# Performance work log

Hardware: AMD Instinct MI355X
Metric: run time of the kernel (lower is better)

Reference implementation:

```python
import jax, jax.numpy as jnp
import numpy as np

# ---- O(2) irrep machinery -------------------------------------------------
# Irrep (m, p): dim = 1 if m == 0 else 2 (real basis (cos m*theta, sin m*theta)).
# Product rules from trig identities; 'component' normalization: cg *= sqrt(dim_out).
R2 = 1.0 / np.sqrt(2.0)

def _cg_paths(m1, p1, m2, p2):
    out = []
    if m1 == 0 and m2 == 0:
        out.append((0, p1 * p2, np.ones((1, 1, 1))))
    elif m1 == 0:
        c = np.zeros((1, 2, 2)); c[0, 0, 0] = 1.0; c[0, 1, 1] = 1.0
        out.append((m2, p1 * p2, c))
    elif m2 == 0:
        c = np.zeros((2, 1, 2)); c[0, 0, 0] = 1.0; c[1, 0, 1] = 1.0
        out.append((m1, p1 * p2, c))
    else:
        if m1 == m2:
            c = np.zeros((2, 2, 1)); c[0, 0, 0] = R2; c[1, 1, 0] = R2  # cos(a-b): scalar
            out.append((0, p1 * p2, c))
            c = np.zeros((2, 2, 1)); c[1, 0, 0] = R2; c[0, 1, 0] = -R2  # sin(a-b): pseudoscalar
            out.append((0, -p1 * p2, c))
        else:
            sgn = 1.0 if m1 > m2 else -1.0
            c = np.zeros((2, 2, 2))
            c[0, 0, 0] = R2; c[1, 1, 0] = R2          # cos(a-b) = cc + ss
            c[1, 0, 1] = sgn * R2; c[0, 1, 1] = -sgn * R2  # sin(a-b) = sc - cs
            out.append((abs(m1 - m2), p1 * p2, c))
        c = np.zeros((2, 2, 2))
        c[0, 0, 0] = R2; c[1, 1, 0] = -R2  # cos(a+b) = cc - ss
        c[1, 0, 1] = R2; c[0, 1, 1] = R2   # sin(a+b) = sc + cs
        out.append((m1 + m2, p1 * p2, c))
    # component normalization
    return [(m, p, (cg * np.sqrt(cg.shape[-1])).astype(np.float32)) for m, p, cg in out]

# (mul, m, parity) -- already regrouped (sorted, deduplicated)
IRREPS1 = [(64, 0, 1), (64, 1, 1), (64, 2, 1), (64, 3, 1)]  # dim 448
IRREPS2 = [(32, 0, 1), (32, 1, 1), (32, 2, 1)]              # dim 160

def _build():
    paths = []
    off1 = 0
    for mul1, m1, p1 in IRREPS1:
        d1 = 1 if m1 == 0 else 2
        off2 = 0
        for mul2, m2, p2 in IRREPS2:
            d2 = 1 if m2 == 0 else 2
            for mo, po, cg in _cg_paths(m1, p1, m2, p2):
                paths.append((off1, mul1, d1, off2, mul2, d2, cg, mo, po))
            off2 += mul2 * d2
        off1 += mul1 * d1
    # stable sort of output chunks by irrep (m, parity) -> irreps_out.sort().inv
    inv = sorted(range(len(paths)), key=lambda i: (paths[i][7], -paths[i][8]))
    return paths, inv

PATHS, INV = _build()
BATCH = 2048
DIM1 = 448
DIM2 = 160


def setup_inputs() -> dict:
    key = jax.random.key(0)
    k1, k2 = jax.random.split(key)
    return {
        "input1": jax.random.normal(k1, (BATCH, DIM1), dtype=jnp.float32),
        "input2": jax.random.normal(k2, (BATCH, DIM2), dtype=jnp.float32),
    }


def reference(input1, input2):
    # inputs already share leading shape and dtype (mirrors _prepare_inputs)
    lead = input1.shape[:-1]
    chunks = []
    for off1, mul1, d1, off2, mul2, d2, cg, _, _ in PATHS:
        x1 = input1[..., off1:off1 + mul1 * d1].reshape(lead + (mul1, d1))
        x2 = input2[..., off2:off2 + mul2 * d2].reshape(lead + (mul2, d2))
        cgj = jnp.asarray(cg, dtype=input1.dtype)  # (d1, d2, d_out), sparse CG
        chunk = jnp.einsum('...ui,...vj,ijk->...uvk', x1, x2, cgj)
        chunks.append(chunk.reshape(lead + (mul1 * mul2 * cg.shape[-1],)))
    return jnp.concatenate([chunks[i] for i in INV], axis=-1)
```

## Files before the change

### kernel.cpp

```cpp
#include <hip/hip_runtime.h>


#define R2F  0.70710678118654752440f
#define SQ2F 1.41421356237309504880f

constexpr int BATCH = 2048;
constexpr int DIM1  = 448;
constexpr int DIM2  = 160;
constexpr int ODIM  = 71680;

__global__ __launch_bounds__(256)
void tp_kernel(const float* __restrict__ g1, const float* __restrict__ g2,
               float* __restrict__ gout) {
    const int b  = blockIdx.x;
    const int t0 = threadIdx.x;

    __shared__ float s1[DIM1];
    __shared__ float s2[DIM2];
    {
        const float* x1 = g1 + (size_t)b * DIM1;
        const float* x2 = g2 + (size_t)b * DIM2;
        for (int i = t0; i < DIM1; i += 256) s1[i] = x1[i];
        for (int i = t0; i < DIM2; i += 256) s2[i] = x2[i];
    }
    __syncthreads();

    float4* out = (float4*)(gout + (size_t)b * ODIM);

    auto chunk_ss = [&](int dst4, const float* a, const float* b) {
#pragma unroll
        for (int r = 0; r < 2; ++r) {
            int t = t0 + r * 256;
            int u = t >> 3;
            int v = (4 * t) & 31;
            float au = a[u];
            out[dst4 + t] = make_float4(au * b[v], au * b[v + 1],
                                        au * b[v + 2], au * b[v + 3]);
        }
    };
    auto chunk_cos = [&](int dst4, const float* a, const float* b) {
#pragma unroll
        for (int r = 0; r < 2; ++r) {
            int t = t0 + r * 256;
            int u = t >> 3;
            int v = (4 * t) & 31;
            float ac = R2F * a[2 * u], as = R2F * a[2 * u + 1];
            float4 res;
            res.x = ac * b[2 * v + 0] + as * b[2 * v + 1];
            res.y = ac * b[2 * v + 2] + as * b[2 * v + 3];
            res.z = ac * b[2 * v + 4] + as * b[2 * v + 5];
            res.w = ac * b[2 * v + 6] + as * b[2 * v + 7];
            out[dst4 + t] = res;
        }
    };
    auto chunk_sin = [&](int dst4, const float* a, const float* b) {
#pragma unroll
        for (int r = 0; r < 2; ++r) {
            int t = t0 + r * 256;
            int u = t >> 3;
            int v = (4 * t) & 31;
            float ac = R2F * a[2 * u], as = R2F * a[2 * u + 1];
            float4 res;
            res.x = as * b[2 * v + 0] - ac * b[2 * v + 1];
            res.y = as * b[2 * v + 2] - ac * b[2 * v + 3];
            res.z = as * b[2 * v + 4] - ac * b[2 * v + 5];
            res.w = as * b[2 * v + 6] - ac * b[2 * v + 7];
            out[dst4 + t] = res;
        }
    };

    auto chunk_sv = [&](int dst4, const float* a, const float* b) {
#pragma unroll
        for (int r = 0; r < 4; ++r) {
            int t = t0 + r * 256;
            int u = t >> 4;
            int v = (2 * t) & 31;
            float au = SQ2F * a[u];
            out[dst4 + t] = make_float4(au * b[2 * v + 0], au * b[2 * v + 1],
                                        au * b[2 * v + 2], au * b[2 * v + 3]);
        }
    };
    auto chunk_vs = [&](int dst4, const float* a, const float* b) {
#pragma unroll
        for (int r = 0; r < 4; ++r) {
            int t = t0 + r * 256;
            int u = t >> 4;
            int v = (2 * t) & 31;
            float ac = SQ2F * a[2 * u], as = SQ2F * a[2 * u + 1];
            out[dst4 + t] = make_float4(ac * b[v], as * b[v],
                                        ac * b[v + 1], as * b[v + 1]);
        }
    };
    auto chunk_sum = [&](int dst4, const float* a, const float* b) {
#pragma unroll
        for (int r = 0; r < 4; ++r) {
            int t = t0 + r * 256;
            int u = t >> 4;
            int v = (2 * t) & 31;
            float ac = a[2 * u], as = a[2 * u + 1];
            float bc0 = b[2 * v + 0], bs0 = b[2 * v + 1];
            float bc1 = b[2 * v + 2], bs1 = b[2 * v + 3];
            out[dst4 + t] = make_float4(ac * bc0 - as * bs0, as * bc0 + ac * bs0,
                                        ac * bc1 - as * bs1, as * bc1 + ac * bs1);
        }
    };
    auto chunk_diff = [&](int dst4, const float* a, const float* b, float sgn) {
#pragma unroll
        for (int r = 0; r < 4; ++r) {
            int t = t0 + r * 256;
            int u = t >> 4;
            int v = (2 * t) & 31;
            float ac = a[2 * u], as = a[2 * u + 1];
            float bc0 = b[2 * v + 0], bs0 = b[2 * v + 1];
            float bc1 = b[2 * v + 2], bs1 = b[2 * v + 3];
            out[dst4 + t] = make_float4(ac * bc0 + as * bs0, sgn * (as * bc0 - ac * bs0),
                                        ac * bc1 + as * bs1, sgn * (as * bc1 - ac * bs1));
        }
    };

    chunk_ss  (    0, s1 +   0, s2 +  0);
    chunk_cos (  512, s1 +  64, s2 + 32);
    chunk_cos ( 1024, s1 + 192, s2 + 96);
    chunk_sin ( 1536, s1 +  64, s2 + 32);
    chunk_sin ( 2048, s1 + 192, s2 + 96);
    chunk_sv  ( 2560, s1 +   0, s2 + 32);
    chunk_vs  ( 3584, s1 +  64, s2 +  0);
    chunk_diff( 4608, s1 +  64, s2 + 96, -1.f);
    chunk_diff( 5632, s1 + 192, s2 + 32, +1.f);
    chunk_diff( 6656, s1 + 320, s2 + 96, +1.f);
    chunk_sv  ( 7680, s1 +   0, s2 + 96);
    chunk_sum ( 8704, s1 +  64, s2 + 32);
    chunk_vs  ( 9728, s1 + 192, s2 +  0);
    chunk_diff(10752, s1 + 320, s2 + 32, +1.f);
    chunk_sum (11776, s1 +  64, s2 + 96);
    chunk_sum (12800, s1 + 192, s2 + 32);
    chunk_vs  (13824, s1 + 320, s2 +  0);
    chunk_sum (14848, s1 + 192, s2 + 96);
    chunk_sum (15872, s1 + 320, s2 + 32);
    chunk_sum (16896, s1 + 320, s2 + 96);
}

extern "C" void kernel_launch(void* const* d_in, const int* in_sizes, int n_in,
                              void* d_out, int out_size, void* d_ws, size_t ws_size,
                              hipStream_t stream) {
    const float* x1 = (const float*)d_in[0];
    const float* x2 = (const float*)d_in[1];
    float* out = (float*)d_out;
    tp_kernel<<<BATCH, 256, 0, stream>>>(x1, x2, out);
}
```

Before: 576.3 us.

## Use nontemporal stores and regroup output chunks by shared input registers

```diff
diff --git a/kernel.cpp b/kernel.cpp
--- a/kernel.cpp
+++ b/kernel.cpp
@@ -8,6 +8,13 @@
 constexpr int DIM1  = 448;
 constexpr int DIM2  = 160;
 constexpr int ODIM  = 71680;
+
+typedef float v4f __attribute__((ext_vector_type(4)));
+
+__device__ __forceinline__ void ntst(v4f* p, float x, float y, float z, float w) {
+    v4f v = {x, y, z, w};
+    __builtin_nontemporal_store(v, p);
+}
 
 __global__ __launch_bounds__(256)
 void tp_kernel(const float* __restrict__ g1, const float* __restrict__ g2,
@@ -25,119 +32,148 @@
     }
     __syncthreads();
 
-    float4* out = (float4*)(gout + (size_t)b * ODIM);
+    v4f* out = (v4f*)(gout + (size_t)b * ODIM);
 
-    auto chunk_ss = [&](int dst4, const float* a, const float* b) {
+    const int us  = t0 >> 3;
+    const int vsc = (4 * t0) & 31;
+    const int vs2 = 2 * vsc;
+    const int uv  = t0 >> 4;
+    const int vv  = (2 * t0) & 31;
+    const int vv2 = 2 * vv;
+
+    {
+        float b0 = s2[vsc], b1 = s2[vsc + 1], b2 = s2[vsc + 2], b3 = s2[vsc + 3];
+        float a0 = s1[us], a1 = s1[us + 32];
+        ntst(out + t0,       a0*b0, a0*b1, a0*b2, a0*b3);
+        ntst(out + t0 + 256, a1*b0, a1*b1, a1*b2, a1*b3);
+    }
+
+    {
+        float av[4];
+#pragma unroll
+        for (int r = 0; r < 4; ++r) av[r] = s1[uv + 16 * r];
+        float p0 = SQ2F * s2[32 + vv2], p1 = SQ2F * s2[33 + vv2],
+              p2 = SQ2F * s2[34 + vv2], p3 = SQ2F * s2[35 + vv2];
+        float q0 = SQ2F * s2[96 + vv2], q1 = SQ2F * s2[97 + vv2],
+              q2 = SQ2F * s2[98 + vv2], q3 = SQ2F * s2[99 + vv2];
+#pragma unroll
+        for (int r = 0; r < 4; ++r) {
+            float a = av[r];
+            ntst(out + 2560 + t0 + 256 * r, a*p0, a*p1, a*p2, a*p3);
+            ntst(out + 7680 + t0 + 256 * r, a*q0, a*q1, a*q2, a*q3);
+        }
+    }
+
+    {
+        float ca[4], sa[4];
+#pragma unroll
+        for (int r = 0; r < 4; ++r) {
+            int j = 64 + 2 * (uv + 16 * r);
+            ca[r] = s1[j]; sa[r] = s1[j + 1];
+        }
+        float b00 = SQ2F * s2[vv], b01 = SQ2F * s2[vv + 1];
+        float b10 = s2[32 + vv2], b11 = s2[33 + vv2],
+              b12 = s2[34 + vv2], b13 = s2[35 + vv2];
+        float b20 = s2[96 + vv2], b21 = s2[97 + vv2],
+              b22 = s2[98 + vv2], b23 = s2[99 + vv2];
+#pragma unroll
+        for (int r = 0; r < 4; ++r) {
+            float c = ca[r], s = sa[r];
+            ntst(out + 3584 + t0 + 256 * r, c*b00, s*b00, c*b01, s*b01);
+            ntst(out + 4608 + t0 + 256 * r,
+                 c*b20 + s*b21, c*b21 - s*b20,
+                 c*b22 + s*b23, c*b23 - s*b22);
+            ntst(out + 8704 + t0 + 256 * r,
+                 c*b10 - s*b11, s*b10 + c*b11,
+                 c*b12 - s*b13, s*b12 + c*b13);
+            ntst(out + 11776 + t0 + 256 * r,
+                 c*b20 - s*b21, s*b20 + c*b21,
+                 c*b22 - s*b23, s*b22 + c*b23);
+        }
+        float e0 = s2[32 + vs2], e1 = s2[33 + vs2], e2 = s2[34 + vs2],
+              e3 = s2[35 + vs2], e4 = s2[36 + vs2], e5 = s2[37 + vs2],
+              e6 = s2[38 + vs2], e7 = s2[39 + vs2];
 #pragma unroll
         for (int r = 0; r < 2; ++r) {
-            int t = t0 + r * 256;
-            int u = t >> 3;
-            int v = (4 * t) & 31;
-            float au = a[u];
-            out[dst4 + t] = make_float4(au * b[v], au * b[v + 1],
-                                        au * b[v + 2], au * b[v + 3]);
+            int j = 64 + 2 * (us + 32 * r);
+            float c = R2F * s1[j], s = R2F * s1[j + 1];
+            ntst(out + 512 + t0 + 256 * r,
+                 c*e0 + s*e1, c*e2 + s*e3, c*e4 + s*e5, c*e6 + s*e7);
+            ntst(out + 1536 + t0 + 256 * r,
+                 s*e0 - c*e1, s*e2 - c*e3, s*e4 - c*e5, s*e6 - c*e7);
         }
-    };
-    auto chunk_cos = [&](int dst4, const float* a, const float* b) {
+    }
+
+    {
+        float ca[4], sa[4];
+#pragma unroll
+        for (int r = 0; r < 4; ++r) {
+            int j = 192 + 2 * (uv + 16 * r);
+            ca[r] = s1[j]; sa[r] = s1[j + 1];
+        }
+        float b00 = SQ2F * s2[vv], b01 = SQ2F * s2[vv + 1];
+        float b10 = s2[32 + vv2], b11 = s2[33 + vv2],
+              b12 = s2[34 + vv2], b13 = s2[35 + vv2];
+        float b20 = s2[96 + vv2], b21 = s2[97 + vv2],
+              b22 = s2[98 + vv2], b23 = s2[99 + vv2];
+#pragma unroll
+        for (int r = 0; r < 4; ++r) {
+            float c = ca[r], s = sa[r];
+            ntst(out + 5632 + t0 + 256 * r,
+                 c*b10 + s*b11, s*b10 - c*b11,
+                 c*b12 + s*b13, s*b12 - c*b13);
+            ntst(out + 9728 + t0 + 256 * r, c*b00, s*b00, c*b01, s*b01);
+            ntst(out + 12800 + t0 + 256 * r,
+                 c*b10 - s*b11, s*b10 + c*b11,
+                 c*b12 - s*b13, s*b12 + c*b13);
+            ntst(out + 14848 + t0 + 256 * r,
+                 c*b20 - s*b21, s*b20 + c*b21,
+                 c*b22 - s*b23, s*b22 + c*b23);
+        }
+        float e0 = s2[96 + vs2], e1 = s2[97 + vs2], e2 = s2[98 + vs2],
+              e3 = s2[99 + vs2], e4 = s2[100 + vs2], e5 = s2[101 + vs2],
+              e6 = s2[102 + vs2], e7 = s2[103 + vs2];
 #pragma unroll
         for (int r = 0; r < 2; ++r) {
-            int t = t0 + r * 256;
-            int u = t >> 3;
-            int v = (4 * t) & 31;
-            float ac = R2F * a[2 * u], as = R2F * a[2 * u + 1];
-            float4 res;
-            res.x = ac * b[2 * v + 0] + as * b[2 * v + 1];
-            res.y = ac * b[2 * v + 2] + as * b[2 * v + 3];
-            res.z = ac * b[2 * v + 4] + as * b[2 * v + 5];
-            res.w = ac * b[2 * v + 6] + as * b[2 * v + 7];
-            out[dst4 + t] = res;
+            int j = 192 + 2 * (us + 32 * r);
+            float c = R2F * s1[j], s = R2F * s1[j + 1];
+            ntst(out + 1024 + t0 + 256 * r,
+                 c*e0 + s*e1, c*e2 + s*e3, c*e4 + s*e5, c*e6 + s*e7);
+            ntst(out + 2048 + t0 + 256 * r,
+                 s*e0 - c*e1, s*e2 - c*e3, s*e4 - c*e5, s*e6 - c*e7);
         }
-    };
-    auto chunk_sin = [&](int dst4, const float* a, const float* b) {
-#pragma unroll
-        for (int r = 0; r < 2; ++r) {
-            int t = t0 + r * 256;
-            int u = t >> 3;
-            int v = (4 * t) & 31;
-            float ac = R2F * a[2 * u], as = R2F * a[2 * u + 1];
-            float4 res;
-            res.x = as * b[2 * v + 0] - ac * b[2 * v + 1];
-            res.y = as * b[2 * v + 2] - ac * b[2 * v + 3];
-            res.z = as * b[2 * v + 4] - ac * b[2 * v + 5];
-            res.w = as * b[2 * v + 6] - ac * b[2 * v + 7];
-            out[dst4 + t] = res;
-        }
-    };
+    }
 
-    auto chunk_sv = [&](int dst4, const float* a, const float* b) {
+    {
+        float ca[4], sa[4];
 #pragma unroll
         for (int r = 0; r < 4; ++r) {
-            int t = t0 + r * 256;
-            int u = t >> 4;
-            int v = (2 * t) & 31;
-            float au = SQ2F * a[u];
-            out[dst4 + t] = make_float4(au * b[2 * v + 0], au * b[2 * v + 1],
-                                        au * b[2 * v + 2], au * b[2 * v + 3]);
+            int j = 320 + 2 * (uv + 16 * r);
+            ca[r] = s1[j]; sa[r] = s1[j + 1];
         }
-    };
-    auto chunk_vs = [&](int dst4, const float* a, const float* b) {
+        float b00 = SQ2F * s2[vv], b01 = SQ2F * s2[vv + 1];
+        float b10 = s2[32 + vv2], b11 = s2[33 + vv2],
+              b12 = s2[34 + vv2], b13 = s2[35 + vv2];
+        float b20 = s2[96 + vv2], b21 = s2[97 + vv2],
+              b22 = s2[98 + vv2], b23 = s2[99 + vv2];
 #pragma unroll
         for (int r = 0; r < 4; ++r) {
-            int t = t0 + r * 256;
-            int u = t >> 4;
-            int v = (2 * t) & 31;
-            float ac = SQ2F * a[2 * u], as = SQ2F * a[2 * u + 1];
-            out[dst4 + t] = make_float4(ac * b[v], as * b[v],
-                                        ac * b[v + 1], as * b[v + 1]);
+            float c = ca[r], s = sa[r];
+            ntst(out + 6656 + t0 + 256 * r,
+                 c*b20 + s*b21, s*b20 - c*b21,
+                 c*b22 + s*b23, s*b22 - c*b23);
+            ntst(out + 10752 + t0 + 256 * r,
+                 c*b10 + s*b11, s*b10 - c*b11,
+                 c*b12 + s*b13, s*b12 - c*b13);
+            ntst(out + 13824 + t0 + 256 * r, c*b00, s*b00, c*b01, s*b01);
+            ntst(out + 15872 + t0 + 256 * r,
+                 c*b10 - s*b11, s*b10 + c*b11,
+                 c*b12 - s*b13, s*b12 + c*b13);
+            ntst(out + 16896 + t0 + 256 * r,
+                 c*b20 - s*b21, s*b20 + c*b21,
+                 c*b22 - s*b23, s*b22 + c*b23);
         }
-    };
-    auto chunk_sum = [&](int dst4, const float* a, const float* b) {
-#pragma unroll
-        for (int r = 0; r < 4; ++r) {
-            int t = t0 + r * 256;
-            int u = t >> 4;
-            int v = (2 * t) & 31;
-            float ac = a[2 * u], as = a[2 * u + 1];
-            float bc0 = b[2 * v + 0], bs0 = b[2 * v + 1];
-            float bc1 = b[2 * v + 2], bs1 = b[2 * v + 3];
-            out[dst4 + t] = make_float4(ac * bc0 - as * bs0, as * bc0 + ac * bs0,
-                                        ac * bc1 - as * bs1, as * bc1 + ac * bs1);
-        }
-    };
-    auto chunk_diff = [&](int dst4, const float* a, const float* b, float sgn) {
-#pragma unroll
-        for (int r = 0; r < 4; ++r) {
-            int t = t0 + r * 256;
-            int u = t >> 4;
-            int v = (2 * t) & 31;
-            float ac = a[2 * u], as = a[2 * u + 1];
-            float bc0 = b[2 * v + 0], bs0 = b[2 * v + 1];
-            float bc1 = b[2 * v + 2], bs1 = b[2 * v + 3];
-            out[dst4 + t] = make_float4(ac * bc0 + as * bs0, sgn * (as * bc0 - ac * bs0),
-                                        ac * bc1 + as * bs1, sgn * (as * bc1 - ac * bs1));
-        }
-    };
-
-    chunk_ss  (    0, s1 +   0, s2 +  0);
-    chunk_cos (  512, s1 +  64, s2 + 32);
-    chunk_cos ( 1024, s1 + 192, s2 + 96);
-    chunk_sin ( 1536, s1 +  64, s2 + 32);
-    chunk_sin ( 2048, s1 + 192, s2 + 96);
-    chunk_sv  ( 2560, s1 +   0, s2 + 32);
-    chunk_vs  ( 3584, s1 +  64, s2 +  0);
-    chunk_diff( 4608, s1 +  64, s2 + 96, -1.f);
-    chunk_diff( 5632, s1 + 192, s2 + 32, +1.f);
-    chunk_diff( 6656, s1 + 320, s2 + 96, +1.f);
-    chunk_sv  ( 7680, s1 +   0, s2 + 96);
-    chunk_sum ( 8704, s1 +  64, s2 + 32);
-    chunk_vs  ( 9728, s1 + 192, s2 +  0);
-    chunk_diff(10752, s1 + 320, s2 + 32, +1.f);
-    chunk_sum (11776, s1 +  64, s2 + 96);
-    chunk_sum (12800, s1 + 192, s2 + 32);
-    chunk_vs  (13824, s1 + 320, s2 +  0);
-    chunk_sum (14848, s1 + 192, s2 + 96);
-    chunk_sum (15872, s1 + 320, s2 + 32);
-    chunk_sum (16896, s1 + 320, s2 + 96);
+    }
 }
 
 extern "C" void kernel_launch(void* const* d_in, const int* in_sizes, int n_in,
```

After: 575.0 us. Within noise of the previous version (-0.2%).

## Split each row into per-piece blocks and use nontemporal stores

Applied to the files above, without the earlier changes.

```diff
diff --git a/kernel.cpp b/kernel.cpp
--- a/kernel.cpp
+++ b/kernel.cpp
@@ -4,140 +4,131 @@
 #define R2F  0.70710678118654752440f
 #define SQ2F 1.41421356237309504880f
 
-constexpr int BATCH = 2048;
-constexpr int DIM1  = 448;
-constexpr int DIM2  = 160;
-constexpr int ODIM  = 71680;
+constexpr int BATCH  = 2048;
+constexpr int DIM1   = 448;
+constexpr int DIM2   = 160;
+constexpr int ODIM   = 71680;
+constexpr int NPIECE = 35;
+
+typedef float v4f __attribute__((ext_vector_type(4)));
+
+__device__ __forceinline__ void ntst(v4f* p, float x, float y, float z, float w) {
+    v4f v = {x, y, z, w};
+    __builtin_nontemporal_store(v, p);
+}
+
+__constant__ const unsigned char PTYPE[NPIECE] = {
+    0, 1, 1, 2, 2,
+    3, 3, 4, 4, 6, 6, 7, 7, 7, 7,
+    3, 3, 5, 5, 4, 4, 7, 7,
+    5, 5, 5, 5, 4, 4,
+    5, 5, 5, 5,
+    5, 5
+};
+__constant__ const short AOFF[NPIECE] = {
+    0, 64, 192, 64, 192,
+    0, 0, 64, 64, 64, 64, 192, 192, 320, 320,
+    0, 0, 64, 64, 192, 192, 320, 320,
+    64, 64, 192, 192, 320, 320,
+    192, 192, 320, 320,
+    320, 320
+};
+__constant__ const short BOFF[NPIECE] = {
+    0, 32, 96, 32, 96,
+    32, 32, 0, 0, 96, 96, 32, 32, 96, 96,
+    96, 96, 32, 32, 0, 0, 32, 32,
+    96, 96, 32, 32, 0, 0,
+    96, 96, 32, 32,
+    96, 96
+};
+__constant__ const short UADD[NPIECE] = {
+    0, 0, 0, 0, 0,
+    0, 32, 0, 32, 0, 32, 0, 32, 0, 32,
+    0, 32, 0, 32, 0, 32, 0, 32,
+    0, 32, 0, 32, 0, 32,
+    0, 32, 0, 32,
+    0, 32
+};
 
 __global__ __launch_bounds__(256)
 void tp_kernel(const float* __restrict__ g1, const float* __restrict__ g2,
                float* __restrict__ gout) {
-    const int b  = blockIdx.x;
-    const int t0 = threadIdx.x;
+    const unsigned g   = blockIdx.x;
+    const unsigned row = g / NPIECE;
+    const int      p   = (int)(g - row * NPIECE);
+    const int      t0  = threadIdx.x;
 
-    __shared__ float s1[DIM1];
-    __shared__ float s2[DIM2];
-    {
-        const float* x1 = g1 + (size_t)b * DIM1;
-        const float* x2 = g2 + (size_t)b * DIM2;
-        for (int i = t0; i < DIM1; i += 256) s1[i] = x1[i];
-        for (int i = t0; i < DIM2; i += 256) s2[i] = x2[i];
+    const float* __restrict__ a  = g1 + (size_t)row * DIM1 + AOFF[p];
+    const float* __restrict__ bp = g2 + (size_t)row * DIM2 + BOFF[p];
+    v4f* out = (v4f*)(gout + (size_t)row * ODIM) + p * 512;
+
+    const int ty = PTYPE[p];
+
+    if (ty <= 2) {
+        const int v = (4 * t0) & 31;
+        const int u = t0 >> 3;
+        if (ty == 0) {
+            float b0 = bp[v], b1 = bp[v + 1], b2 = bp[v + 2], b3 = bp[v + 3];
+            float a0 = a[u], a1 = a[u + 32];
+            ntst(out + t0,       a0 * b0, a0 * b1, a0 * b2, a0 * b3);
+            ntst(out + t0 + 256, a1 * b0, a1 * b1, a1 * b2, a1 * b3);
+        } else {
+            const int v2 = 2 * v;
+            float e0 = bp[v2],     e1 = bp[v2 + 1], e2 = bp[v2 + 2], e3 = bp[v2 + 3],
+                  e4 = bp[v2 + 4], e5 = bp[v2 + 5], e6 = bp[v2 + 6], e7 = bp[v2 + 7];
+            float c0 = R2F * a[2 * u],        s0 = R2F * a[2 * u + 1];
+            float c1 = R2F * a[2 * u + 64],   s1 = R2F * a[2 * u + 65];
+            if (ty == 1) {
+                ntst(out + t0,       c0*e0 + s0*e1, c0*e2 + s0*e3,
+                                     c0*e4 + s0*e5, c0*e6 + s0*e7);
+                ntst(out + t0 + 256, c1*e0 + s1*e1, c1*e2 + s1*e3,
+                                     c1*e4 + s1*e5, c1*e6 + s1*e7);
+            } else {
+                ntst(out + t0,       s0*e0 - c0*e1, s0*e2 - c0*e3,
+                                     s0*e4 - c0*e5, s0*e6 - c0*e7);
+                ntst(out + t0 + 256, s1*e0 - c1*e1, s1*e2 - c1*e3,
+                                     s1*e4 - c1*e5, s1*e6 - c1*e7);
+            }
+        }
+    } else {
+        const int vI = (2 * t0) & 31;
+        const int v2 = 2 * vI;
+        const int u0 = UADD[p] + (t0 >> 4);
+        const int u1 = u0 + 16;
+        if (ty == 3) {
+            float b0 = SQ2F * bp[v2],     b1 = SQ2F * bp[v2 + 1],
+                  b2 = SQ2F * bp[v2 + 2], b3 = SQ2F * bp[v2 + 3];
+            float a0 = a[u0], a1 = a[u1];
+            ntst(out + t0,       a0 * b0, a0 * b1, a0 * b2, a0 * b3);
+            ntst(out + t0 + 256, a1 * b0, a1 * b1, a1 * b2, a1 * b3);
+        } else if (ty == 4) {
+            float bv0 = bp[vI], bv1 = bp[vI + 1];
+            float c0 = SQ2F * a[2 * u0], s0 = SQ2F * a[2 * u0 + 1];
+            float c1 = SQ2F * a[2 * u1], s1 = SQ2F * a[2 * u1 + 1];
+            ntst(out + t0,       c0 * bv0, s0 * bv0, c0 * bv1, s0 * bv1);
+            ntst(out + t0 + 256, c1 * bv0, s1 * bv0, c1 * bv1, s1 * bv1);
+        } else {
+            float bc0 = bp[v2], bs0 = bp[v2 + 1], bc1 = bp[v2 + 2], bs1 = bp[v2 + 3];
+            float c0 = a[2 * u0], s0 = a[2 * u0 + 1];
+            float c1 = a[2 * u1], s1 = a[2 * u1 + 1];
+            if (ty == 5) {
+                ntst(out + t0,
+                     c0*bc0 - s0*bs0, s0*bc0 + c0*bs0,
+                     c0*bc1 - s0*bs1, s0*bc1 + c0*bs1);
+                ntst(out + t0 + 256,
+                     c1*bc0 - s1*bs0, s1*bc0 + c1*bs0,
+                     c1*bc1 - s1*bs1, s1*bc1 + c1*bs1);
+            } else {
+                const float sgn = (ty == 6) ? -1.f : 1.f;
+                ntst(out + t0,
+                     c0*bc0 + s0*bs0, sgn * (s0*bc0 - c0*bs0),
+                     c0*bc1 + s0*bs1, sgn * (s0*bc1 - c0*bs1));
+                ntst(out + t0 + 256,
+                     c1*bc0 + s1*bs0, sgn * (s1*bc0 - c1*bs0),
+                     c1*bc1 + s1*bs1, sgn * (s1*bc1 - c1*bs1));
+            }
+        }
     }
-    __syncthreads();
-
-    float4* out = (float4*)(gout + (size_t)b * ODIM);
-
-    auto chunk_ss = [&](int dst4, const float* a, const float* b) {
-#pragma unroll
-        for (int r = 0; r < 2; ++r) {
-            int t = t0 + r * 256;
-            int u = t >> 3;
-            int v = (4 * t) & 31;
-            float au = a[u];
-            out[dst4 + t] = make_float4(au * b[v], au * b[v + 1],
-                                        au * b[v + 2], au * b[v + 3]);
-        }
-    };
-    auto chunk_cos = [&](int dst4, const float* a, const float* b) {
-#pragma unroll
-        for (int r = 0; r < 2; ++r) {
-            int t = t0 + r * 256;
-            int u = t >> 3;
-            int v = (4 * t) & 31;
-            float ac = R2F * a[2 * u], as = R2F * a[2 * u + 1];
-            float4 res;
-            res.x = ac * b[2 * v + 0] + as * b[2 * v + 1];
-            res.y = ac * b[2 * v + 2] + as * b[2 * v + 3];
-            res.z = ac * b[2 * v + 4] + as * b[2 * v + 5];
-            res.w = ac * b[2 * v + 6] + as * b[2 * v + 7];
-            out[dst4 + t] = res;
-        }
-    };
-    auto chunk_sin = [&](int dst4, const float* a, const float* b) {
-#pragma unroll
-        for (int r = 0; r < 2; ++r) {
-            int t = t0 + r * 256;
-            int u = t >> 3;
-            int v = (4 * t) & 31;
-            float ac = R2F * a[2 * u], as = R2F * a[2 * u + 1];
-            float4 res;
-            res.x = as * b[2 * v + 0] - ac * b[2 * v + 1];
-            res.y = as * b[2 * v + 2] - ac * b[2 * v + 3];
-            res.z = as * b[2 * v + 4] - ac * b[2 * v + 5];
-            res.w = as * b[2 * v + 6] - ac * b[2 * v + 7];
-            out[dst4 + t] = res;
-        }
-    };
-
-    auto chunk_sv = [&](int dst4, const float* a, const float* b) {
-#pragma unroll
-        for (int r = 0; r < 4; ++r) {
-            int t = t0 + r * 256;
-            int u = t >> 4;
-            int v = (2 * t) & 31;
-            float au = SQ2F * a[u];
-            out[dst4 + t] = make_float4(au * b[2 * v + 0], au * b[2 * v + 1],
-                                        au * b[2 * v + 2], au * b[2 * v + 3]);
-        }
-    };
-    auto chunk_vs = [&](int dst4, const float* a, const float* b) {
-#pragma unroll
-        for (int r = 0; r < 4; ++r) {
-            int t = t0 + r * 256;
-            int u = t >> 4;
-            int v = (2 * t) & 31;
-            float ac = SQ2F * a[2 * u], as = SQ2F * a[2 * u + 1];
-            out[dst4 + t] = make_float4(ac * b[v], as * b[v],
-                                        ac * b[v + 1], as * b[v + 1]);
-        }
-    };
-    auto chunk_sum = [&](int dst4, const float* a, const float* b) {
-#pragma unroll
-        for (int r = 0; r < 4; ++r) {
-            int t = t0 + r * 256;
-            int u = t >> 4;
-            int v = (2 * t) & 31;
-            float ac = a[2 * u], as = a[2 * u + 1];
-            float bc0 = b[2 * v + 0], bs0 = b[2 * v + 1];
-            float bc1 = b[2 * v + 2], bs1 = b[2 * v + 3];
-            out[dst4 + t] = make_float4(ac * bc0 - as * bs0, as * bc0 + ac * bs0,
-                                        ac * bc1 - as * bs1, as * bc1 + ac * bs1);
-        }
-    };
-    auto chunk_diff = [&](int dst4, const float* a, const float* b, float sgn) {
-#pragma unroll
-        for (int r = 0; r < 4; ++r) {
-            int t = t0 + r * 256;
-            int u = t >> 4;
-            int v = (2 * t) & 31;
-            float ac = a[2 * u], as = a[2 * u + 1];
-            float bc0 = b[2 * v + 0], bs0 = b[2 * v + 1];
-            float bc1 = b[2 * v + 2], bs1 = b[2 * v + 3];
-            out[dst4 + t] = make_float4(ac * bc0 + as * bs0, sgn * (as * bc0 - ac * bs0),
-                                        ac * bc1 + as * bs1, sgn * (as * bc1 - ac * bs1));
-        }
-    };
-
-    chunk_ss  (    0, s1 +   0, s2 +  0);
-    chunk_cos (  512, s1 +  64, s2 + 32);
-    chunk_cos ( 1024, s1 + 192, s2 + 96);
-    chunk_sin ( 1536, s1 +  64, s2 + 32);
-    chunk_sin ( 2048, s1 + 192, s2 + 96);
-    chunk_sv  ( 2560, s1 +   0, s2 + 32);
-    chunk_vs  ( 3584, s1 +  64, s2 +  0);
-    chunk_diff( 4608, s1 +  64, s2 + 96, -1.f);
-    chunk_diff( 5632, s1 + 192, s2 + 32, +1.f);
-    chunk_diff( 6656, s1 + 320, s2 + 96, +1.f);
-    chunk_sv  ( 7680, s1 +   0, s2 + 96);
-    chunk_sum ( 8704, s1 +  64, s2 + 32);
-    chunk_vs  ( 9728, s1 + 192, s2 +  0);
-    chunk_diff(10752, s1 + 320, s2 + 32, +1.f);
-    chunk_sum (11776, s1 +  64, s2 + 96);
-    chunk_sum (12800, s1 + 192, s2 + 32);
-    chunk_vs  (13824, s1 + 320, s2 +  0);
-    chunk_sum (14848, s1 + 192, s2 + 96);
-    chunk_sum (15872, s1 + 320, s2 + 32);
-    chunk_sum (16896, s1 + 320, s2 + 96);
 }
 
 extern "C" void kernel_launch(void* const* d_in, const int* in_sizes, int n_in,
@@ -146,5 +137,5 @@
     const float* x1 = (const float*)d_in[0];
     const float* x2 = (const float*)d_in[1];
     float* out = (float*)d_out;
-    tp_kernel<<<BATCH, 256, 0, stream>>>(x1, x2, out);
+    tp_kernel<<<BATCH * NPIECE, 256, 0, stream>>>(x1, x2, out);
 }
```

Measured after the change: 593.2 us. 2.9% more time.
